# Optimization experiments

Measured on AMD Instinct MI355X. Metric: run time of the kernel, lower is better.

Reference implementation:

```python
import jax, jax.numpy as jnp
import numpy as np

N_NODES = 100000
N_EDGES = 1600000
N_GRAPHS = 2000
N_FEAT = 128
HIDDEN = 128
N_LAYERS = 4
BN_EPS = 1e-5


def setup_inputs() -> dict:
    key = jax.random.key(0)
    ks = jax.random.split(key, 8)
    x = jax.random.normal(ks[0], (N_NODES, N_FEAT), dtype=jnp.float32)
    edge_index = jax.random.randint(ks[1], (2, N_EDGES), 0, N_NODES, dtype=jnp.int32)
    batch = jnp.sort(jax.random.randint(ks[2], (N_NODES,), 0, N_GRAPHS, dtype=jnp.int32))
    # layer weights scaled down to keep activations stable over 4 layers
    Ws = jax.random.normal(ks[3], (N_LAYERS, HIDDEN, HIDDEN), dtype=jnp.float32) * 0.1
    bs = jnp.zeros((N_LAYERS, HIDDEN), jnp.float32)
    gammas = jnp.ones((N_LAYERS, HIDDEN), jnp.float32)
    betas = jnp.zeros((N_LAYERS, HIDDEN), jnp.float32)
    run_mean = jnp.zeros((N_LAYERS, HIDDEN), jnp.float32)
    run_var = jnp.ones((N_LAYERS, HIDDEN), jnp.float32)
    W_out = jax.random.normal(ks[4], (HIDDEN, 5), dtype=jnp.float32) * 0.1
    b_out = jnp.zeros((5,), jnp.float32)
    return {"x": x, "edge_index": edge_index, "batch": batch, "Ws": Ws, "bs": bs,
            "gammas": gammas, "betas": betas, "run_mean": run_mean, "run_var": run_var,
            "W_out": W_out, "b_out": b_out}


def _gcn_conv(x, src, dst, norm, self_coef, W, b):
    xw = x @ W                                        # [N, H]
    coef = norm[src] * norm[dst]                      # [E]
    msgs = xw[src] * coef[:, None]                    # [E, H] gather
    agg = jax.ops.segment_sum(msgs, dst, num_segments=N_NODES)  # scatter-add
    agg = agg + xw * self_coef[:, None]               # self-loop term
    return agg + b


def reference(x, edge_index, batch, Ws, bs, gammas, betas, run_mean, run_var, W_out, b_out):
    src, dst = edge_index[0], edge_index[1]
    # degree (incl. self-loop) from destination index
    deg = jax.ops.segment_sum(jnp.ones((N_EDGES,), x.dtype), dst, num_segments=N_NODES) + 1.0
    norm = jax.lax.rsqrt(deg)
    self_coef = norm * norm
    h = x
    for l in range(N_LAYERS):
        h = _gcn_conv(h, src, dst, norm, self_coef, Ws[l], bs[l])
        # BatchNorm1d in eval mode (running stats); dropout is identity in eval
        h = (h - run_mean[l]) * (gammas[l] * jax.lax.rsqrt(run_var[l] + BN_EPS)) + betas[l]
        h = jax.nn.relu(h)
    # global mean pool over graphs
    sums = jax.ops.segment_sum(h, batch, num_segments=N_GRAPHS)
    counts = jax.ops.segment_sum(jnp.ones((N_NODES,), h.dtype), batch, num_segments=N_GRAPHS)
    pooled = sums / jnp.maximum(counts, 1.0)[:, None]  # [G, H]
    return pooled @ W_out + b_out                      # [G, 5]
```

## Files before the change

kernel.cpp:

```cpp
#include <hip/hip_runtime.h>
#include <hip/hip_fp16.h>

#define N_NODES_C 100000
#define N_EDGES_C 1600000
#define N_GRAPHS_C 2000
#define HID 128
#define BN_EPS_C 1e-5f
#define NBUCK 391
#define PART_TILE 4096

typedef _Float16 half8 __attribute__((ext_vector_type(8)));
typedef float float4v __attribute__((ext_vector_type(4)));


__global__ __launch_bounds__(256) void kb_hist(const int* __restrict__ dst, int* __restrict__ bcount) {
    __shared__ int hist[NBUCK];
    const int t = threadIdx.x;
    for (int b = t; b < NBUCK; b += 256) hist[b] = 0;
    __syncthreads();
    const int e0 = blockIdx.x * PART_TILE;
    #pragma unroll
    for (int k = 0; k < 16; k++) {
        int e = e0 + k * 256 + t;
        if (e < N_EDGES_C) atomicAdd(&hist[dst[e] >> 8], 1);
    }
    __syncthreads();
    for (int b = t; b < NBUCK; b += 256) {
        int c = hist[b];
        if (c) atomicAdd(&bcount[b], c);
    }
}

__global__ __launch_bounds__(512) void kb_scan(const int* __restrict__ bcount,
                                               int* __restrict__ bbase, int* __restrict__ bcursor) {
    __shared__ int s[512];
    const int t = threadIdx.x;
    int v = (t < NBUCK) ? bcount[t] : 0;
    s[t] = v;
    __syncthreads();
    for (int off = 1; off < 512; off <<= 1) {
        int u = (t >= off) ? s[t - off] : 0;
        __syncthreads();
        s[t] += u;
        __syncthreads();
    }
    if (t < NBUCK) { int e = s[t] - v; bbase[t] = e; bcursor[t] = e; }
    if (t == 0) bbase[NBUCK] = N_EDGES_C;
}

__global__ __launch_bounds__(256) void kb_part(const int* __restrict__ src, const int* __restrict__ dst,
                                               int* __restrict__ bcursor, int2* __restrict__ ebuf) {
    __shared__ int hist[NBUCK];
    __shared__ int startA[NBUCK];
    __shared__ int lcur[NBUCK];
    const int t = threadIdx.x;
    for (int b = t; b < NBUCK; b += 256) { hist[b] = 0; lcur[b] = 0; }
    __syncthreads();
    const int e0 = blockIdx.x * PART_TILE;
    #pragma unroll
    for (int k = 0; k < 16; k++) {
        int e = e0 + k * 256 + t;
        if (e < N_EDGES_C) atomicAdd(&hist[dst[e] >> 8], 1);
    }
    __syncthreads();
    for (int b = t; b < NBUCK; b += 256) {
        int c = hist[b];
        startA[b] = c ? atomicAdd(&bcursor[b], c) : 0;
    }
    __syncthreads();
    #pragma unroll
    for (int k = 0; k < 16; k++) {
        int e = e0 + k * 256 + t;
        if (e < N_EDGES_C) {
            int d = dst[e];
            int b = d >> 8;
            int pos = startA[b] + atomicAdd(&lcur[b], 1);
            ebuf[pos] = make_int2(src[e], d);
        }
    }
}

__global__ __launch_bounds__(256) void kb_fill(const int2* __restrict__ ebuf, const int* __restrict__ bbase,
                                               int* __restrict__ csr_src, int* __restrict__ offs,
                                               float* __restrict__ norm) {
    __shared__ int s[256];
    __shared__ int excl[256];
    __shared__ int lcur[256];
    const int b = blockIdx.x, t = threadIdx.x;
    const int base = b << 8;
    const int e0 = bbase[b], e1 = bbase[b + 1];
    s[t] = 0; lcur[t] = 0;
    __syncthreads();
    for (int e = e0 + t; e < e1; e += 256)
        atomicAdd(&s[ebuf[e].y & 255], 1);
    __syncthreads();
    int own = s[t];
    for (int off = 1; off < 256; off <<= 1) {
        int v = (t >= off) ? s[t - off] : 0;
        __syncthreads();
        s[t] += v;
        __syncthreads();
    }
    excl[t] = s[t] - own;
    int node = base + t;
    if (node < N_NODES_C) {
        offs[node] = e0 + (s[t] - own);
        norm[node] = rsqrtf((float)own + 1.0f);
    }
    if (b == 0 && t == 0) offs[N_NODES_C] = N_EDGES_C;
    __syncthreads();
    for (int e = e0 + t; e < e1; e += 256) {
        int2 p = ebuf[e];
        int l = p.y & 255;
        int pos = e0 + excl[l] + atomicAdd(&lcur[l], 1);
        csr_src[pos] = p.x;
    }
}


__global__ __launch_bounds__(256) void k_tw(const float* __restrict__ Ws_all, _Float16* __restrict__ WT) {
    int idx = blockIdx.x * 256 + threadIdx.x;
    int l = idx >> 14, r = idx & 16383, k = r >> 7, n = r & 127;
    WT[l * 16384 + n * HID + k] = (_Float16)Ws_all[idx];
}


template<bool F32A>
__global__ __launch_bounds__(256) void k_gemm(const void* __restrict__ Ap,
                                              const _Float16* __restrict__ WT,
                                              const float* __restrict__ norm,
                                              _Float16* __restrict__ Y, int nrows) {
    __shared__ _Float16 Wt[HID][136];
    const int tid = threadIdx.x;
    #pragma unroll
    for (int t = 0; t < 8; t++) {
        int off = tid * 8 + t * 2048;
        half8 v = *(const half8*)&WT[off];
        *(half8*)&Wt[off >> 7][off & 127] = v;
    }
    __syncthreads();

    const int wave = tid >> 6, lane = tid & 63, quad = lane >> 4, l16 = lane & 15;
    half8 Wf[2][4];
    #pragma unroll
    for (int c = 0; c < 2; c++)
        #pragma unroll
        for (int ks = 0; ks < 4; ks++)
            Wf[c][ks] = *(const half8*)&Wt[(wave * 2 + c) * 16 + l16][ks * 32 + quad * 8];

    const int nbase = blockIdx.x * 128;
    #pragma unroll
    for (int t = 0; t < 8; t++) {
        int node = nbase + t * 16 + l16;
        bool ok = node < nrows;
        half8 Af[4];
        if (F32A) {
            const float* arow = (const float*)Ap + (long)node * HID;
            #pragma unroll
            for (int ks = 0; ks < 4; ks++) {
                if (ok) {
                    float4 fa = *(const float4*)&arow[ks * 32 + quad * 8];
                    float4 fb = *(const float4*)&arow[ks * 32 + quad * 8 + 4];
                    _Float16 pk[8] = {(_Float16)fa.x, (_Float16)fa.y, (_Float16)fa.z, (_Float16)fa.w,
                                      (_Float16)fb.x, (_Float16)fb.y, (_Float16)fb.z, (_Float16)fb.w};
                    Af[ks] = *(half8*)pk;
                } else Af[ks] = half8{};
            }
        } else {
            const _Float16* arow = (const _Float16*)Ap + (long)node * HID;
            #pragma unroll
            for (int ks = 0; ks < 4; ks++)
                Af[ks] = ok ? *(const half8*)&arow[ks * 32 + quad * 8] : half8{};
        }
        float4v a0 = {0.f, 0.f, 0.f, 0.f}, a1 = {0.f, 0.f, 0.f, 0.f};
        #pragma unroll
        for (int ks = 0; ks < 4; ks++) {
            a0 = __builtin_amdgcn_mfma_f32_16x16x32_f16(Wf[0][ks], Af[ks], a0, 0, 0, 0);
            a1 = __builtin_amdgcn_mfma_f32_16x16x32_f16(Wf[1][ks], Af[ks], a1, 0, 0, 0);
        }
        float nv = ok ? norm[node] : 0.f;
        _Float16 p0[4], p1[4];
        #pragma unroll
        for (int r = 0; r < 4; r++) {
            p0[r] = (_Float16)(a0[r] * nv);
            p1[r] = (_Float16)(a1[r] * nv);
        }
        *(ushort4*)&Y[(long)node * HID + (wave * 2 + 0) * 16 + quad * 4] = *(ushort4*)p0;
        *(ushort4*)&Y[(long)node * HID + (wave * 2 + 1) * 16 + quad * 4] = *(ushort4*)p1;
    }
}


__global__ __launch_bounds__(256) void k_agg(const __half* __restrict__ y, const int* __restrict__ offs,
                                             const int* __restrict__ csr_src, const float* __restrict__ norm,
                                             const float* __restrict__ bias, const float* __restrict__ mean,
                                             const float* __restrict__ gamma, const float* __restrict__ var,
                                             const float* __restrict__ beta, __half* __restrict__ h) {
    const int wave = __builtin_amdgcn_readfirstlane(threadIdx.x >> 6);
    const int lane = threadIdx.x & 63;
    const int i = blockIdx.x * 4 + wave;
    const int j = lane * 2;

    float2 f = __half22float2(*(const __half2*)&y[(long)i * HID + j]);
    float acc0 = f.x, acc1 = f.y;

    const int e0 = offs[i], e1 = offs[i + 1];
    int e = e0;
    int id[16];
    #pragma unroll
    for (int u = 0; u < 16; u++) {
        int raw = csr_src[e + u];
        id[u] = (e + u < e1) ? raw : N_NODES_C;
    }
    while (true) {
        const int en = e + 16;
        const bool more = en < e1;
        int idn[16];
        if (more) {
            #pragma unroll
            for (int u = 0; u < 16; u++) {
                int raw = csr_src[en + u];
                idn[u] = (en + u < e1) ? raw : N_NODES_C;
            }
        }
        #pragma unroll
        for (int u = 0; u < 16; u++) {
            float2 g = __half22float2(*(const __half2*)&y[(long)id[u] * HID + j]);
            acc0 += g.x; acc1 += g.y;
        }
        if (!more) break;
        #pragma unroll
        for (int u = 0; u < 16; u++) id[u] = idn[u];
        e = en;
    }

    const float ni = norm[i];
    float2 bi = *(const float2*)&bias[j];
    float2 me = *(const float2*)&mean[j];
    float2 ga = *(const float2*)&gamma[j];
    float2 va = *(const float2*)&var[j];
    float2 be = *(const float2*)&beta[j];
    float v0 = (acc0 * ni + bi.x - me.x) * (ga.x * rsqrtf(va.x + BN_EPS_C)) + be.x;
    float v1 = (acc1 * ni + bi.y - me.y) * (ga.y * rsqrtf(va.y + BN_EPS_C)) + be.y;
    *(__half2*)&h[(long)i * HID + j] = __floats2half2_rn(fmaxf(v0, 0.f), fmaxf(v1, 0.f));
}


__global__ __launch_bounds__(128) void k_pool(const __half* __restrict__ h, const int* __restrict__ batch,
                                              float* __restrict__ psum, int* __restrict__ pcount) {
    const int j = threadIdx.x;
    const int i0 = blockIdx.x * 128;
    const int iend = min(i0 + 128, N_NODES_C);
    if (i0 >= N_NODES_C) return;
    float acc = 0.f;
    int cur = batch[i0];
    int runStart = i0;
    for (int i = i0; i < iend; i++) {
        int g = batch[i];
        if (g != cur) {
            atomicAdd(&psum[(long)cur * HID + j], acc);
            if (j == 0) atomicAdd(&pcount[cur], i - runStart);
            acc = 0.f; cur = g; runStart = i;
        }
        acc += __half2float(h[(long)i * HID + j]);
    }
    atomicAdd(&psum[(long)cur * HID + j], acc);
    if (j == 0) atomicAdd(&pcount[cur], iend - runStart);
}

__global__ __launch_bounds__(128) void k_final(const float* __restrict__ psum, const int* __restrict__ pcount,
                                               const float* __restrict__ W_out, const float* __restrict__ b_out,
                                               float* __restrict__ out) {
    __shared__ float red[128][5];
    const int g = blockIdx.x, j = threadIdx.x;
    float cnt = fmaxf((float)pcount[g], 1.f);
    float p = psum[(long)g * HID + j] / cnt;
    #pragma unroll
    for (int o = 0; o < 5; o++) red[j][o] = p * W_out[j * 5 + o];
    __syncthreads();
    for (int off = 64; off >= 1; off >>= 1) {
        if (j < off) {
            #pragma unroll
            for (int o = 0; o < 5; o++) red[j][o] += red[j + off][o];
        }
        __syncthreads();
    }
    if (j < 5) out[g * 5 + j] = red[0][j] + b_out[j];
}


extern "C" void kernel_launch(void* const* d_in, const int* in_sizes, int n_in,
                              void* d_out, int out_size, void* d_ws, size_t ws_size,
                              hipStream_t stream) {
    const float* x        = (const float*)d_in[0];
    const int*   eidx     = (const int*)d_in[1];
    const int*   src      = eidx;
    const int*   dst      = eidx + N_EDGES_C;
    const int*   batch    = (const int*)d_in[2];
    const float* Ws_all   = (const float*)d_in[3];
    const float* bs       = (const float*)d_in[4];
    const float* gammas   = (const float*)d_in[5];
    const float* betas    = (const float*)d_in[6];
    const float* run_mean = (const float*)d_in[7];
    const float* run_var  = (const float*)d_in[8];
    const float* W_out    = (const float*)d_in[9];
    const float* b_out    = (const float*)d_in[10];
    float* out = (float*)d_out;

    char* wp = (char*)d_ws;
    auto alloc = [&](size_t bytes) { char* p = wp; wp += (bytes + 255) & ~(size_t)255; return p; };
    __half*   h       = (__half*)alloc((size_t)N_NODES_C * HID * 2);
    _Float16* y       = (_Float16*)alloc((size_t)(N_NODES_C + 128) * HID * 2);
    int2*     ebuf    = (int2*)y;
    _Float16* WT      = (_Float16*)alloc((size_t)4 * HID * HID * 2);
    int*      csr_src = (int*)alloc((size_t)(N_EDGES_C + 16) * 4);
    int*      offs    = (int*)alloc((size_t)(N_NODES_C + 1) * 4);
    float*    norm    = (float*)alloc((size_t)N_NODES_C * 4);
    char*     zbeg    = wp;
    float*    psum    = (float*)alloc((size_t)N_GRAPHS_C * HID * 4);
    int*      pcount  = (int*)alloc((size_t)N_GRAPHS_C * 4);
    int*      bcount  = (int*)alloc((NBUCK + 1) * 4);
    size_t    zlen    = (size_t)(wp - zbeg);
    int*      bbase   = (int*)alloc((NBUCK + 1) * 4);
    int*      bcursor = (int*)alloc((NBUCK + 1) * 4);

    hipMemsetAsync(zbeg, 0, zlen, stream);

    k_tw<<<256, 256, 0, stream>>>(Ws_all, WT);

    const int PB = (N_EDGES_C + PART_TILE - 1) / PART_TILE;
    kb_hist<<<PB, 256, 0, stream>>>(dst, bcount);
    kb_scan<<<1, 512, 0, stream>>>(bcount, bbase, bcursor);
    kb_part<<<PB, 256, 0, stream>>>(src, dst, bcursor, ebuf);
    kb_fill<<<NBUCK, 256, 0, stream>>>(ebuf, bbase, csr_src, offs, norm);

    const int GB = (N_NODES_C + 127) / 128;
    const int AB = (N_NODES_C + 3) / 4;
    for (int l = 0; l < 4; l++) {
        const void* A = (l == 0) ? (const void*)x : (const void*)h;
        if (l == 0)
            k_gemm<true><<<GB, 256, 0, stream>>>(A, WT, norm, y, N_NODES_C);
        else
            k_gemm<false><<<GB, 256, 0, stream>>>(A, WT + (size_t)l * HID * HID, norm, y, N_NODES_C);
        k_agg<<<AB, 256, 0, stream>>>((const __half*)y, offs, csr_src, norm,
                                      bs + l * HID, run_mean + l * HID, gammas + l * HID,
                                      run_var + l * HID, betas + l * HID, (__half*)h);
    }
    k_pool <<<GB, 128, 0, stream>>>((const __half*)h, batch, psum, pcount);
    k_final<<<N_GRAPHS_C, 128, 0, stream>>>(psum, pcount, W_out, b_out, out);
}
```

Before: 534.3 us.

## Build CSR with global atomic degree count and scatter; simplify agg loop; finer pooling

Replaces the two-level bucketed radix partition (hist, scan, partition into ebuf, per-bucket fill) with a direct per-node degree count via global atomics, a two-level prefix scan, and an atomic-cursor scatter of source ids into CSR. The aggregation kernel drops its software-prefetch double buffering of neighbor ids in favor of a simple do-while loop. Pooling uses 32-node blocks instead of 128 to raise parallelism. The goals are fewer passes and less intermediate traffic during CSR construction, in exchange for global atomic contention and a non-deterministic neighbor order within each node, which changes float summation order.

```diff
diff --git a/kernel.cpp b/kernel.cpp
--- a/kernel.cpp
+++ b/kernel.cpp
@@ -7,35 +7,42 @@
 #define HID 128
 #define BN_EPS_C 1e-5f
 #define NBUCK 391
-#define PART_TILE 4096
 
 typedef _Float16 half8 __attribute__((ext_vector_type(8)));
 typedef float float4v __attribute__((ext_vector_type(4)));
 
 
-__global__ __launch_bounds__(256) void kb_hist(const int* __restrict__ dst, int* __restrict__ bcount) {
-    __shared__ int hist[NBUCK];
+__global__ __launch_bounds__(256) void k_deg(const int* __restrict__ dst, int* __restrict__ deg) {
+    const int base = blockIdx.x * 1024 + threadIdx.x;
+    #pragma unroll
+    for (int k = 0; k < 4; k++) {
+        int e = base + k * 256;
+        if (e < N_EDGES_C) atomicAdd(&deg[dst[e]], 1);
+    }
+}
+
+__global__ __launch_bounds__(256) void k_scan1(const int* __restrict__ deg,
+                                               int* __restrict__ offs_local, int* __restrict__ btot) {
+    __shared__ int s[256];
     const int t = threadIdx.x;
-    for (int b = t; b < NBUCK; b += 256) hist[b] = 0;
+    const int node = blockIdx.x * 256 + t;
+    int v = (node < N_NODES_C) ? deg[node] : 0;
+    s[t] = v;
     __syncthreads();
-    const int e0 = blockIdx.x * PART_TILE;
-    #pragma unroll
-    for (int k = 0; k < 16; k++) {
-        int e = e0 + k * 256 + t;
-        if (e < N_EDGES_C) atomicAdd(&hist[dst[e] >> 8], 1);
-    }
-    __syncthreads();
-    for (int b = t; b < NBUCK; b += 256) {
-        int c = hist[b];
-        if (c) atomicAdd(&bcount[b], c);
-    }
-}
-
-__global__ __launch_bounds__(512) void kb_scan(const int* __restrict__ bcount,
-                                               int* __restrict__ bbase, int* __restrict__ bcursor) {
+    for (int off = 1; off < 256; off <<= 1) {
+        int u = (t >= off) ? s[t - off] : 0;
+        __syncthreads();
+        s[t] += u;
+        __syncthreads();
+    }
+    if (node < N_NODES_C) offs_local[node] = s[t] - v;
+    if (t == 255) btot[blockIdx.x] = s[255];
+}
+
+__global__ __launch_bounds__(512) void k_scan2(const int* __restrict__ btot, int* __restrict__ bbase) {
     __shared__ int s[512];
     const int t = threadIdx.x;
-    int v = (t < NBUCK) ? bcount[t] : 0;
+    int v = (t < NBUCK) ? btot[t] : 0;
     s[t] = v;
     __syncthreads();
     for (int off = 1; off < 512; off <<= 1) {
@@ -44,76 +51,32 @@
         s[t] += u;
         __syncthreads();
     }
-    if (t < NBUCK) { int e = s[t] - v; bbase[t] = e; bcursor[t] = e; }
-    if (t == 0) bbase[NBUCK] = N_EDGES_C;
-}
-
-__global__ __launch_bounds__(256) void kb_part(const int* __restrict__ src, const int* __restrict__ dst,
-                                               int* __restrict__ bcursor, int2* __restrict__ ebuf) {
-    __shared__ int hist[NBUCK];
-    __shared__ int startA[NBUCK];
-    __shared__ int lcur[NBUCK];
-    const int t = threadIdx.x;
-    for (int b = t; b < NBUCK; b += 256) { hist[b] = 0; lcur[b] = 0; }
-    __syncthreads();
-    const int e0 = blockIdx.x * PART_TILE;
-    #pragma unroll
-    for (int k = 0; k < 16; k++) {
-        int e = e0 + k * 256 + t;
-        if (e < N_EDGES_C) atomicAdd(&hist[dst[e] >> 8], 1);
-    }
-    __syncthreads();
-    for (int b = t; b < NBUCK; b += 256) {
-        int c = hist[b];
-        startA[b] = c ? atomicAdd(&bcursor[b], c) : 0;
-    }
-    __syncthreads();
-    #pragma unroll
-    for (int k = 0; k < 16; k++) {
-        int e = e0 + k * 256 + t;
+    if (t < NBUCK) bbase[t] = s[t] - v;
+}
+
+__global__ __launch_bounds__(256) void k_fix(const int* __restrict__ deg, const int* __restrict__ offs_local,
+                                             const int* __restrict__ bbase, int* __restrict__ offs,
+                                             int* __restrict__ cursor, float* __restrict__ norm) {
+    const int node = blockIdx.x * 256 + threadIdx.x;
+    if (node < N_NODES_C) {
+        int o = bbase[node >> 8] + offs_local[node];
+        offs[node] = o;
+        cursor[node] = o;
+        norm[node] = rsqrtf((float)deg[node] + 1.0f);
+    }
+    if (node == 0) offs[N_NODES_C] = N_EDGES_C;
+}
+
+__global__ __launch_bounds__(256) void k_scatter(const int* __restrict__ src, const int* __restrict__ dst,
+                                                 int* __restrict__ cursor, int* __restrict__ csr_src) {
+    const int base = blockIdx.x * 1024 + threadIdx.x;
+    #pragma unroll
+    for (int k = 0; k < 4; k++) {
+        int e = base + k * 256;
         if (e < N_EDGES_C) {
-            int d = dst[e];
-            int b = d >> 8;
-            int pos = startA[b] + atomicAdd(&lcur[b], 1);
-            ebuf[pos] = make_int2(src[e], d);
-        }
-    }
-}
-
-__global__ __launch_bounds__(256) void kb_fill(const int2* __restrict__ ebuf, const int* __restrict__ bbase,
-                                               int* __restrict__ csr_src, int* __restrict__ offs,
-                                               float* __restrict__ norm) {
-    __shared__ int s[256];
-    __shared__ int excl[256];
-    __shared__ int lcur[256];
-    const int b = blockIdx.x, t = threadIdx.x;
-    const int base = b << 8;
-    const int e0 = bbase[b], e1 = bbase[b + 1];
-    s[t] = 0; lcur[t] = 0;
-    __syncthreads();
-    for (int e = e0 + t; e < e1; e += 256)
-        atomicAdd(&s[ebuf[e].y & 255], 1);
-    __syncthreads();
-    int own = s[t];
-    for (int off = 1; off < 256; off <<= 1) {
-        int v = (t >= off) ? s[t - off] : 0;
-        __syncthreads();
-        s[t] += v;
-        __syncthreads();
-    }
-    excl[t] = s[t] - own;
-    int node = base + t;
-    if (node < N_NODES_C) {
-        offs[node] = e0 + (s[t] - own);
-        norm[node] = rsqrtf((float)own + 1.0f);
-    }
-    if (b == 0 && t == 0) offs[N_NODES_C] = N_EDGES_C;
-    __syncthreads();
-    for (int e = e0 + t; e < e1; e += 256) {
-        int2 p = ebuf[e];
-        int l = p.y & 255;
-        int pos = e0 + excl[l] + atomicAdd(&lcur[l], 1);
-        csr_src[pos] = p.x;
+            int pos = atomicAdd(&cursor[dst[e]], 1);
+            csr_src[pos] = src[e];
+        }
     }
 }
 
@@ -206,33 +169,20 @@
 
     const int e0 = offs[i], e1 = offs[i + 1];
     int e = e0;
-    int id[16];
-    #pragma unroll
-    for (int u = 0; u < 16; u++) {
-        int raw = csr_src[e + u];
-        id[u] = (e + u < e1) ? raw : N_NODES_C;
-    }
-    while (true) {
-        const int en = e + 16;
-        const bool more = en < e1;
-        int idn[16];
-        if (more) {
-            #pragma unroll
-            for (int u = 0; u < 16; u++) {
-                int raw = csr_src[en + u];
-                idn[u] = (en + u < e1) ? raw : N_NODES_C;
-            }
+    do {
+        int id[16];
+        #pragma unroll
+        for (int u = 0; u < 16; u++) {
+            int raw = csr_src[e + u];
+            id[u] = (e + u < e1) ? raw : N_NODES_C;
         }
         #pragma unroll
         for (int u = 0; u < 16; u++) {
             float2 g = __half22float2(*(const __half2*)&y[(long)id[u] * HID + j]);
             acc0 += g.x; acc1 += g.y;
         }
-        if (!more) break;
-        #pragma unroll
-        for (int u = 0; u < 16; u++) id[u] = idn[u];
-        e = en;
-    }
+        e += 16;
+    } while (e < e1);
 
     const float ni = norm[i];
     float2 bi = *(const float2*)&bias[j];
@@ -249,8 +199,8 @@
 __global__ __launch_bounds__(128) void k_pool(const __half* __restrict__ h, const int* __restrict__ batch,
                                               float* __restrict__ psum, int* __restrict__ pcount) {
     const int j = threadIdx.x;
-    const int i0 = blockIdx.x * 128;
-    const int iend = min(i0 + 128, N_NODES_C);
+    const int i0 = blockIdx.x * 32;
+    const int iend = min(i0 + 32, N_NODES_C);
     if (i0 >= N_NODES_C) return;
     float acc = 0.f;
     int cur = batch[i0];
@@ -309,30 +259,32 @@
 
     char* wp = (char*)d_ws;
     auto alloc = [&](size_t bytes) { char* p = wp; wp += (bytes + 255) & ~(size_t)255; return p; };
-    __half*   h       = (__half*)alloc((size_t)N_NODES_C * HID * 2);
-    _Float16* y       = (_Float16*)alloc((size_t)(N_NODES_C + 128) * HID * 2);
-    int2*     ebuf    = (int2*)y;
-    _Float16* WT      = (_Float16*)alloc((size_t)4 * HID * HID * 2);
-    int*      csr_src = (int*)alloc((size_t)(N_EDGES_C + 16) * 4);
-    int*      offs    = (int*)alloc((size_t)(N_NODES_C + 1) * 4);
-    float*    norm    = (float*)alloc((size_t)N_NODES_C * 4);
-    char*     zbeg    = wp;
-    float*    psum    = (float*)alloc((size_t)N_GRAPHS_C * HID * 4);
-    int*      pcount  = (int*)alloc((size_t)N_GRAPHS_C * 4);
-    int*      bcount  = (int*)alloc((NBUCK + 1) * 4);
-    size_t    zlen    = (size_t)(wp - zbeg);
-    int*      bbase   = (int*)alloc((NBUCK + 1) * 4);
-    int*      bcursor = (int*)alloc((NBUCK + 1) * 4);
+    __half*   h        = (__half*)alloc((size_t)N_NODES_C * HID * 2);
+    _Float16* y        = (_Float16*)alloc((size_t)(N_NODES_C + 128) * HID * 2);
+    _Float16* WT       = (_Float16*)alloc((size_t)4 * HID * HID * 2);
+    int*      csr_src  = (int*)alloc((size_t)(N_EDGES_C + 16) * 4);
+    int*      offs     = (int*)alloc((size_t)(N_NODES_C + 1) * 4);
+    float*    norm     = (float*)alloc((size_t)N_NODES_C * 4);
+    int*      offs_loc = (int*)alloc((size_t)N_NODES_C * 4);
+    int*      cursor   = (int*)alloc((size_t)N_NODES_C * 4);
+    int*      btot     = (int*)alloc((NBUCK + 1) * 4);
+    int*      bbase    = (int*)alloc((NBUCK + 1) * 4);
+    char*     zbeg     = wp;
+    float*    psum     = (float*)alloc((size_t)N_GRAPHS_C * HID * 4);
+    int*      pcount   = (int*)alloc((size_t)N_GRAPHS_C * 4);
+    int*      deg      = (int*)alloc((size_t)N_NODES_C * 4);
+    size_t    zlen     = (size_t)(wp - zbeg);
 
     hipMemsetAsync(zbeg, 0, zlen, stream);
 
     k_tw<<<256, 256, 0, stream>>>(Ws_all, WT);
 
-    const int PB = (N_EDGES_C + PART_TILE - 1) / PART_TILE;
-    kb_hist<<<PB, 256, 0, stream>>>(dst, bcount);
-    kb_scan<<<1, 512, 0, stream>>>(bcount, bbase, bcursor);
-    kb_part<<<PB, 256, 0, stream>>>(src, dst, bcursor, ebuf);
-    kb_fill<<<NBUCK, 256, 0, stream>>>(ebuf, bbase, csr_src, offs, norm);
+    const int EB = (N_EDGES_C + 1023) / 1024;
+    k_deg    <<<EB, 256, 0, stream>>>(dst, deg);
+    k_scan1  <<<NBUCK, 256, 0, stream>>>(deg, offs_loc, btot);
+    k_scan2  <<<1, 512, 0, stream>>>(btot, bbase);
+    k_fix    <<<NBUCK, 256, 0, stream>>>(deg, offs_loc, bbase, offs, cursor, norm);
+    k_scatter<<<EB, 256, 0, stream>>>(src, dst, cursor, csr_src);
 
     const int GB = (N_NODES_C + 127) / 128;
     const int AB = (N_NODES_C + 3) / 4;
@@ -346,6 +298,7 @@
                                       bs + l * HID, run_mean + l * HID, gammas + l * HID,
                                       run_var + l * HID, betas + l * HID, (__half*)h);
     }
-    k_pool <<<GB, 128, 0, stream>>>((const __half*)h, batch, psum, pcount);
+    const int PB2 = (N_NODES_C + 31) / 32;
+    k_pool <<<PB2, 128, 0, stream>>>((const __half*)h, batch, psum, pcount);
     k_final<<<N_GRAPHS_C, 128, 0, stream>>>(psum, pcount, W_out, b_out, out);
 }
```

Result: slower. 641.8 us (+20.1%).

## Pack edge buffer to 32-bit, drop aggregation prefetch, shrink pool tiles

Applied to the files above, without the earlier changes.

The bucketed edge partition now stores each edge as one int, (src<<8)|(dst&255), instead of an int2, which halves the write and read traffic of the intermediate buffer. The aggregation kernel drops its software double-buffered index prefetch for a simpler do-while loop, which lowers register pressure but no longer overlaps index loads with gathers. The pooling kernel processes 32 nodes per block instead of 128, giving more blocks for parallelism at the cost of more atomics. The packing relies on src fitting in 24 bits, which holds for 100k nodes.

```diff
diff --git a/kernel.cpp b/kernel.cpp
--- a/kernel.cpp
+++ b/kernel.cpp
@@ -49,7 +49,7 @@
 }
 
 __global__ __launch_bounds__(256) void kb_part(const int* __restrict__ src, const int* __restrict__ dst,
-                                               int* __restrict__ bcursor, int2* __restrict__ ebuf) {
+                                               int* __restrict__ bcursor, int* __restrict__ ebuf) {
     __shared__ int hist[NBUCK];
     __shared__ int startA[NBUCK];
     __shared__ int lcur[NBUCK];
@@ -75,12 +75,12 @@
             int d = dst[e];
             int b = d >> 8;
             int pos = startA[b] + atomicAdd(&lcur[b], 1);
-            ebuf[pos] = make_int2(src[e], d);
-        }
-    }
-}
-
-__global__ __launch_bounds__(256) void kb_fill(const int2* __restrict__ ebuf, const int* __restrict__ bbase,
+            ebuf[pos] = (src[e] << 8) | (d & 255);
+        }
+    }
+}
+
+__global__ __launch_bounds__(256) void kb_fill(const int* __restrict__ ebuf, const int* __restrict__ bbase,
                                                int* __restrict__ csr_src, int* __restrict__ offs,
                                                float* __restrict__ norm) {
     __shared__ int s[256];
@@ -92,7 +92,7 @@
     s[t] = 0; lcur[t] = 0;
     __syncthreads();
     for (int e = e0 + t; e < e1; e += 256)
-        atomicAdd(&s[ebuf[e].y & 255], 1);
+        atomicAdd(&s[ebuf[e] & 255], 1);
     __syncthreads();
     int own = s[t];
     for (int off = 1; off < 256; off <<= 1) {
@@ -110,10 +110,10 @@
     if (b == 0 && t == 0) offs[N_NODES_C] = N_EDGES_C;
     __syncthreads();
     for (int e = e0 + t; e < e1; e += 256) {
-        int2 p = ebuf[e];
-        int l = p.y & 255;
+        int p = ebuf[e];
+        int l = p & 255;
         int pos = e0 + excl[l] + atomicAdd(&lcur[l], 1);
-        csr_src[pos] = p.x;
+        csr_src[pos] = p >> 8;
     }
 }
 
@@ -206,33 +206,20 @@
 
     const int e0 = offs[i], e1 = offs[i + 1];
     int e = e0;
-    int id[16];
-    #pragma unroll
-    for (int u = 0; u < 16; u++) {
-        int raw = csr_src[e + u];
-        id[u] = (e + u < e1) ? raw : N_NODES_C;
-    }
-    while (true) {
-        const int en = e + 16;
-        const bool more = en < e1;
-        int idn[16];
-        if (more) {
-            #pragma unroll
-            for (int u = 0; u < 16; u++) {
-                int raw = csr_src[en + u];
-                idn[u] = (en + u < e1) ? raw : N_NODES_C;
-            }
+    do {
+        int id[16];
+        #pragma unroll
+        for (int u = 0; u < 16; u++) {
+            int raw = csr_src[e + u];
+            id[u] = (e + u < e1) ? raw : N_NODES_C;
         }
         #pragma unroll
         for (int u = 0; u < 16; u++) {
             float2 g = __half22float2(*(const __half2*)&y[(long)id[u] * HID + j]);
             acc0 += g.x; acc1 += g.y;
         }
-        if (!more) break;
-        #pragma unroll
-        for (int u = 0; u < 16; u++) id[u] = idn[u];
-        e = en;
-    }
+        e += 16;
+    } while (e < e1);
 
     const float ni = norm[i];
     float2 bi = *(const float2*)&bias[j];
@@ -249,8 +236,8 @@
 __global__ __launch_bounds__(128) void k_pool(const __half* __restrict__ h, const int* __restrict__ batch,
                                               float* __restrict__ psum, int* __restrict__ pcount) {
     const int j = threadIdx.x;
-    const int i0 = blockIdx.x * 128;
-    const int iend = min(i0 + 128, N_NODES_C);
+    const int i0 = blockIdx.x * 32;
+    const int iend = min(i0 + 32, N_NODES_C);
     if (i0 >= N_NODES_C) return;
     float acc = 0.f;
     int cur = batch[i0];
@@ -311,18 +298,18 @@
     auto alloc = [&](size_t bytes) { char* p = wp; wp += (bytes + 255) & ~(size_t)255; return p; };
     __half*   h       = (__half*)alloc((size_t)N_NODES_C * HID * 2);
     _Float16* y       = (_Float16*)alloc((size_t)(N_NODES_C + 128) * HID * 2);
-    int2*     ebuf    = (int2*)y;
+    int*      ebuf    = (int*)y;
     _Float16* WT      = (_Float16*)alloc((size_t)4 * HID * HID * 2);
     int*      csr_src = (int*)alloc((size_t)(N_EDGES_C + 16) * 4);
     int*      offs    = (int*)alloc((size_t)(N_NODES_C + 1) * 4);
     float*    norm    = (float*)alloc((size_t)N_NODES_C * 4);
+    int*      bbase   = (int*)alloc((NBUCK + 1) * 4);
+    int*      bcursor = (int*)alloc((NBUCK + 1) * 4);
     char*     zbeg    = wp;
     float*    psum    = (float*)alloc((size_t)N_GRAPHS_C * HID * 4);
     int*      pcount  = (int*)alloc((size_t)N_GRAPHS_C * 4);
     int*      bcount  = (int*)alloc((NBUCK + 1) * 4);
     size_t    zlen    = (size_t)(wp - zbeg);
-    int*      bbase   = (int*)alloc((NBUCK + 1) * 4);
-    int*      bcursor = (int*)alloc((NBUCK + 1) * 4);
 
     hipMemsetAsync(zbeg, 0, zlen, stream);
 
@@ -346,6 +333,7 @@
                                       bs + l * HID, run_mean + l * HID, gammas + l * HID,
                                       run_var + l * HID, betas + l * HID, (__half*)h);
     }
-    k_pool <<<GB, 128, 0, stream>>>((const __half*)h, batch, psum, pcount);
+    const int PB2 = (N_NODES_C + 31) / 32;
+    k_pool <<<PB2, 128, 0, stream>>>((const __half*)h, batch, psum, pcount);
     k_final<<<N_GRAPHS_C, 128, 0, stream>>>(psum, pcount, W_out, b_out, out);
 }
```

Result: faster. 502.0 us (-6.0%).
